# Kernel tuning notes

Measured on AMD Instinct MI355X. Metric: run time of the kernel, lower is better.

The kernel has to match this reference:

```python
import jax, jax.numpy as jnp
import numpy as np

NW, NT, F, H = 8192, 4096, 128, 128


def setup_inputs() -> dict:
    key = jax.random.key(0)
    ks = jax.random.split(key, 16)
    s = 1.0 / np.sqrt(F)
    sh = 1.0 / np.sqrt(H)
    inp = {
        "raw_worker_x": jax.random.normal(ks[0], (NW, F), jnp.float32),
        "raw_task_x": jax.random.normal(ks[1], (NT, F), jnp.float32),
        # sparse binary adjacencies (p=0.01), stored dense as the module expects
        "ww_adj": (jax.random.uniform(ks[2], (NW, NW)) < 0.01).astype(jnp.float32),
        "wt_adj": (jax.random.uniform(ks[3], (NW, NT)) < 0.01).astype(jnp.float32),
        # projections (Linear with bias), stored [in, out]
        "Wp_w": jax.random.uniform(ks[4], (F, H), jnp.float32, -s, s),
        "bp_w": jax.random.uniform(ks[5], (H,), jnp.float32, -s, s),
        "Wp_t": jax.random.uniform(ks[6], (F, H), jnp.float32, -s, s),
        "bp_t": jax.random.uniform(ks[7], (H,), jnp.float32, -s, s),
        # RGCN layer
        "W_worker": jax.random.uniform(ks[8], (H, H), jnp.float32, -sh, sh),
        "b_worker": jax.random.uniform(ks[9], (H,), jnp.float32, -sh, sh),
        "W_task": jax.random.uniform(ks[10], (H, H), jnp.float32, -sh, sh),
        "b_task": jax.random.uniform(ks[11], (H,), jnp.float32, -sh, sh),
        "W_ww": jax.random.uniform(ks[12], (H, H), jnp.float32, -sh, sh),
        "W_wt": jax.random.uniform(ks[13], (H, H), jnp.float32, -sh, sh),
        "W_tw": jax.random.uniform(ks[14], (H, H), jnp.float32, -sh, sh),
        # IGAT layer
        "W_igat": jax.random.uniform(ks[15], (H, H), jnp.float32, -sh, sh),
        "a_src": jax.random.normal(jax.random.fold_in(key, 100), (H, 1), jnp.float32) * 0.1,
        "a_dst": jax.random.normal(jax.random.fold_in(key, 101), (H, 1), jnp.float32) * 0.1,
    }
    return inp


def reference(raw_worker_x, raw_task_x, ww_adj, wt_adj,
              Wp_w, bp_w, Wp_t, bp_t,
              W_worker, b_worker, W_task, b_task,
              W_ww, W_wt, W_tw, W_igat, a_src, a_dst):
    # input projections
    h_w = jax.nn.relu(raw_worker_x @ Wp_w + bp_w)   # [NW, H]
    h_t = jax.nn.relu(raw_task_x @ Wp_t + bp_t)     # [NT, H]

    # HeteroRGCN layer
    ww_msg = ww_adj @ (h_w @ W_ww)                  # [NW, H]
    tw_msg = wt_adj @ (h_t @ W_tw)                  # [NW, H]
    wt_msg = wt_adj.T @ (h_w @ W_wt)                # [NT, H]
    h_w_rgcn = jax.nn.relu(h_w @ W_worker + b_worker + ww_msg + tw_msg)
    h_t_rgcn = jax.nn.relu(h_t @ W_task + b_task + wt_msg)

    # IGAT layer: dense masked attention over worker-worker graph
    Wh = h_w_rgcn @ W_igat                          # [NW, H]
    f_src = Wh @ a_src                              # [NW, 1]
    f_dst = Wh @ a_dst                              # [NW, 1]
    e = jax.nn.leaky_relu(f_src + f_dst.T, 0.2)     # [NW, NW]
    NEG = jnp.float32(-9e15)
    attn_logits = jnp.where(ww_adj > 0, e, NEG)
    attention = jax.nn.softmax(attn_logits, axis=-1)
    h_prime = jax.nn.elu(attention @ Wh)            # [NW, H]

    final_worker = h_prime + h_w
    final_task = h_t_rgcn + h_t
    return (final_worker, final_task)
```

## Files before the change

### kernel.cpp

```cpp
#include <hip/hip_runtime.h>

static constexpr int NWK  = 8192;
static constexpr int NTK  = 4096;
static constexpr int HD   = 128;
static constexpr int CWW  = 256;
static constexpr int CWTR = 128;
static constexpr int CWTC = 256;

typedef float  f32x4  __attribute__((ext_vector_type(4)));
typedef __bf16 bf16x8 __attribute__((ext_vector_type(8)));

__device__ __forceinline__ float b2f(unsigned short u){
  unsigned int x = ((unsigned int)u) << 16;
  return __builtin_bit_cast(float, x);
}
__device__ __forceinline__ unsigned short f2b(float x){
  return __builtin_bit_cast(unsigned short, (__bf16)x);
}
__device__ __forceinline__ float wredmax(float v){
#pragma unroll
  for(int o=32;o;o>>=1) v = fmaxf(v, __shfl_xor(v,o,64));
  return v;
}
__device__ __forceinline__ float wredsum(float v){
#pragma unroll
  for(int o=32;o;o>>=1) v += __shfl_xor(v,o,64);
  return v;
}

__global__ __launch_bounds__(256) void prepw(
    const float* s0,const float* s1,const float* s2,const float* s3,
    const float* s4,const float* s5,const float* s6,const float* s7,
    unsigned short* dst, int* fill, float* whsum){
  if(blockIdx.x < 16) fill[blockIdx.x*256 + threadIdx.x] = 0;
  if(blockIdx.x == 16 && threadIdx.x < 128) whsum[threadIdx.x] = 0.f;
  const float* srcs[8] = {s0,s1,s2,s3,s4,s5,s6,s7};
  int mat = blockIdx.x>>2, sl = blockIdx.x&3;
  const float* s = srcs[mat];
  unsigned short* d = dst + (size_t)mat*HD*HD;
  for(int idx=threadIdx.x + sl*4096; idx<(sl+1)*4096; idx+=256){
    int k = idx>>7, n = idx&127;
    d[n*HD+k] = f2b(s[idx]);
  }
}

template<int CAP>
__device__ __forceinline__ void scan_chunk(
    float4 x, int c0base, int& base, int* __restrict__ sbuf, int lane){
  bool p0=x.x>0.f, p1=x.y>0.f, p2=x.z>0.f, p3=x.w>0.f;
  unsigned long long b0=__ballot(p0),b1=__ballot(p1),b2=__ballot(p2),b3=__ballot(p3);
  unsigned long long below = (1ull<<lane)-1ull;
  int pos = base + __popcll(b0&below)+__popcll(b1&below)+__popcll(b2&below)+__popcll(b3&below);
  int c0 = c0base + lane*4;
  if(p0){ if(pos<CAP) sbuf[pos]=c0;   pos++; }
  if(p1){ if(pos<CAP) sbuf[pos]=c0+1; pos++; }
  if(p2){ if(pos<CAP) sbuf[pos]=c0+2; pos++; }
  if(p3){ if(pos<CAP) sbuf[pos]=c0+3; pos++; }
  base += __popcll(b0)+__popcll(b1)+__popcll(b2)+__popcll(b3);
}

template<bool SCATTER, int CAP>
__device__ __forceinline__ void scan_row(
    const float* __restrict__ adj, long row, int ncols,
    int* __restrict__ orow, int* __restrict__ deg,
    int* __restrict__ cidx, int* __restrict__ fill, int ccap,
    int lane, int* __restrict__ sbuf){
  const float4* arow = (const float4*)(adj + row*(long)ncols);
  int base = 0;
  const int nit = ncols>>10;
  float4 v[4], nv[4];
#pragma unroll
  for(int c=0;c<4;c++) v[c] = arow[c*64 + lane];
  for(int it=0; it<nit-1; it++){
#pragma unroll
    for(int c=0;c<4;c++) nv[c] = arow[(it+1)*256 + c*64 + lane];
#pragma unroll
    for(int c=0;c<4;c++)
      scan_chunk<CAP>(v[c], it*1024 + c*256, base, sbuf, lane);
#pragma unroll
    for(int c=0;c<4;c++) v[c] = nv[c];
  }
#pragma unroll
  for(int c=0;c<4;c++)
    scan_chunk<CAP>(v[c], (nit-1)*1024 + c*256, base, sbuf, lane);

  int d = base<CAP ? base : CAP;
  if(lane==0) deg[row] = d;
  if(CAP == 256){
    int4 q = ((const int4*)sbuf)[lane];
    ((int4*)orow)[lane] = q;
  } else {
    int2 q = ((const int2*)sbuf)[lane];
    ((int2*)orow)[lane] = q;
  }
  if(SCATTER){
    for(int k=lane; k<d; k+=64){
      int task = sbuf[k];
      int pp = atomicAdd(&fill[task], 1);
      if(pp < ccap) cidx[(long)task*ccap + pp] = (int)row;
    }
  }
}

__global__ __launch_bounds__(256) void build_all(
    const float* __restrict__ WW, const float* __restrict__ WT,
    int* __restrict__ ww_idx, int* __restrict__ ww_deg,
    int* __restrict__ wt_idx, int* __restrict__ wt_deg,
    int* __restrict__ cidx, int* __restrict__ fill){
  __shared__ int sbuf[4][CWW];
  int lane = threadIdx.x&63, w = threadIdx.x>>6;
  int b = blockIdx.x;
  if(b < NWK/4){
    long row = (long)b*4 + w;
    scan_row<false,CWW>(WW, row, NWK, ww_idx + row*CWW, ww_deg,
                        nullptr, nullptr, 0, lane, sbuf[w]);
  } else {
    long row = (long)(b - NWK/4)*4 + w;
    scan_row<true,CWTR>(WT, row, NTK, wt_idx + row*CWTR, wt_deg,
                        cidx, fill, CWTC, lane, sbuf[w]);
  }
}

__global__ __launch_bounds__(256) void kproj(
    const float* __restrict__ Xw, const float* __restrict__ Xt,
    const unsigned short* __restrict__ Wtb,
    const float* __restrict__ bp_w, const float* __restrict__ bp_t,
    unsigned short* __restrict__ h_w, unsigned short* __restrict__ h_t){
  bool task = blockIdx.x >= (NWK/32);
  const float* X = task ? Xt : Xw;
  const __bf16* Wt = (const __bf16*)(Wtb + (size_t)(task?1:0)*HD*HD);
  const float* bias = task ? bp_t : bp_w;
  unsigned short* H = task ? h_t : h_w;
  long r0 = (long)(task ? blockIdx.x-(NWK/32) : blockIdx.x)*32;

  __shared__ __bf16 As[32*HD];
  char* Ab = (char*)As;
  int t = threadIdx.x, lane = t&63, w = t>>6;
  const float4* A4 = (const float4*)(X + r0*HD);
#pragma unroll
  for(int i=0;i<4;i++){
    int id = t + i*256;
    float4 v = A4[id];
    int row = id>>5, c4 = id&31;
    int byte = row*256 + c4*8;
    ushort4 b; b.x=f2b(v.x); b.y=f2b(v.y); b.z=f2b(v.z); b.w=f2b(v.w);
    *(ushort4*)(Ab + (byte ^ ((row&7)<<4))) = b;
  }
  __syncthreads();
  f32x4 acc[2][2] = {};
  int n0 = w*32;
#pragma unroll
  for(int kk=0;kk<4;kk++){
    int kb = kk*32 + (lane>>4)*8;
    bf16x8 bf0 = *(const bf16x8*)(Wt + (n0 +      (lane&15))*HD + kb);
    bf16x8 bf1 = *(const bf16x8*)(Wt + (n0 + 16 + (lane&15))*HD + kb);
#pragma unroll
    for(int m=0;m<2;m++){
      int row = m*16 + (lane&15);
      bf16x8 af = *(const bf16x8*)(Ab + ((row*256 + kb*2) ^ ((row&7)<<4)));
      acc[m][0] = __builtin_amdgcn_mfma_f32_16x16x32_bf16(af, bf0, acc[m][0], 0,0,0);
      acc[m][1] = __builtin_amdgcn_mfma_f32_16x16x32_bf16(af, bf1, acc[m][1], 0,0,0);
    }
  }
#pragma unroll
  for(int m=0;m<2;m++)
#pragma unroll
  for(int n=0;n<2;n++){
    int col = n0 + n*16 + (lane&15);
    float bc = bias[col];
#pragma unroll
    for(int i=0;i<4;i++){
      long row = r0 + m*16 + (lane>>4)*4 + i;
      float vv = acc[m][n][i] + bc;
      vv = vv>0.f ? vv : 0.f;
      H[row*HD+col] = f2b(vv);
    }
  }
}

__device__ __forceinline__ void gather_sum(
    const unsigned short* __restrict__ tab, const int* __restrict__ ji, int d,
    int lane, float& ax, float& ay){
  int k=0;
  for(; k+3<d; k+=4){
    long j0=ji[k], j1=ji[k+1], j2=ji[k+2], j3=ji[k+3];
    ushort2 u0 = *(const ushort2*)(tab + j0*HD + lane*2);
    ushort2 u1 = *(const ushort2*)(tab + j1*HD + lane*2);
    ushort2 u2 = *(const ushort2*)(tab + j2*HD + lane*2);
    ushort2 u3 = *(const ushort2*)(tab + j3*HD + lane*2);
    ax += (b2f(u0.x)+b2f(u1.x)) + (b2f(u2.x)+b2f(u3.x));
    ay += (b2f(u0.y)+b2f(u1.y)) + (b2f(u2.y)+b2f(u3.y));
  }
  for(; k<d; ++k){
    long j0=ji[k];
    ushort2 u0 = *(const ushort2*)(tab + j0*HD + lane*2);
    ax += b2f(u0.x); ay += b2f(u0.y);
  }
}

__global__ __launch_bounds__(256) void agg(
    const unsigned short* __restrict__ h_w, const unsigned short* __restrict__ h_t,
    const int* __restrict__ wwidx, const int* __restrict__ wwdeg,
    const int* __restrict__ wtidx, const int* __restrict__ wtdeg,
    const int* __restrict__ cidx,  const int* __restrict__ fill,
    unsigned short* __restrict__ g_ww, unsigned short* __restrict__ g_tw,
    unsigned short* __restrict__ g_wt){
  int w = threadIdx.x>>6, lane = threadIdx.x&63;
  long i = (long)blockIdx.x*4 + w;
  if(i < NWK){
    float ax=0.f, ay=0.f;
    gather_sum(h_w, wwidx + i*CWW, wwdeg[i], lane, ax, ay);
    ushort2 o; o.x=f2b(ax); o.y=f2b(ay);
    *(ushort2*)(g_ww + i*HD + lane*2) = o;
    ax=0.f; ay=0.f;
    gather_sum(h_t, wtidx + i*CWTR, wtdeg[i], lane, ax, ay);
    o.x=f2b(ax); o.y=f2b(ay);
    *(ushort2*)(g_tw + i*HD + lane*2) = o;
  } else {
    long tt = i - NWK;
    float ax=0.f, ay=0.f;
    int d = fill[tt]; if(d>CWTC) d=CWTC;
    gather_sum(h_w, cidx + tt*CWTC, d, lane, ax, ay);
    ushort2 o; o.x=f2b(ax); o.y=f2b(ay);
    *(ushort2*)(g_wt + tt*HD + lane*2) = o;
  }
}

__device__ __forceinline__ void stage_bf16(char* Ab, const unsigned short* src, int t){
#pragma unroll
  for(int i=0;i<2;i++){
    int id = t + i*256;
    int row = id>>4, c8 = id&15;
    bf16x8 v = *(const bf16x8*)(src + row*HD + c8*8);
    int byte = row*256 + c8*16;
    *(bf16x8*)(Ab + (byte ^ ((row&7)<<4))) = v;
  }
}

__global__ __launch_bounds__(256) void krgcn(
    const unsigned short* __restrict__ h_w, const unsigned short* __restrict__ h_t,
    const unsigned short* __restrict__ g_ww, const unsigned short* __restrict__ g_tw,
    const unsigned short* __restrict__ g_wt,
    const unsigned short* __restrict__ Wtb,
    const float* __restrict__ b_worker, const float* __restrict__ b_task,
    const float* __restrict__ a_src, const float* __restrict__ a_dst,
    unsigned short* __restrict__ Wh, float* __restrict__ fs, float* __restrict__ fd,
    float* __restrict__ whsum, float* __restrict__ out_task){
  __shared__ __bf16 As[3][32*HD];
  __shared__ __bf16 Hs[32*HD];
  __shared__ float fsp[32][4], fdp[32][4];
  int t = threadIdx.x, lane = t&63, w = t>>6, n0 = w*32;
  bool task = blockIdx.x >= (NWK/32);

  if(!task){
    long r0 = (long)blockIdx.x*32;
    stage_bf16((char*)As[0], h_w  + r0*HD, t);
    stage_bf16((char*)As[1], g_ww + r0*HD, t);
    stage_bf16((char*)As[2], g_tw + r0*HD, t);
    __syncthreads();
    f32x4 acc[2][2] = {};
    const int slot[3] = {2,4,6};
#pragma unroll
    for(int s=0;s<3;s++){
      const __bf16* Wt = (const __bf16*)(Wtb + (size_t)slot[s]*HD*HD);
      char* Ab = (char*)As[s];
#pragma unroll
      for(int kk=0;kk<4;kk++){
        int kb = kk*32 + (lane>>4)*8;
        bf16x8 bf0 = *(const bf16x8*)(Wt + (n0 +      (lane&15))*HD + kb);
        bf16x8 bf1 = *(const bf16x8*)(Wt + (n0 + 16 + (lane&15))*HD + kb);
#pragma unroll
        for(int m=0;m<2;m++){
          int row = m*16 + (lane&15);
          bf16x8 af = *(const bf16x8*)(Ab + ((row*256 + kb*2) ^ ((row&7)<<4)));
          acc[m][0] = __builtin_amdgcn_mfma_f32_16x16x32_bf16(af, bf0, acc[m][0], 0,0,0);
          acc[m][1] = __builtin_amdgcn_mfma_f32_16x16x32_bf16(af, bf1, acc[m][1], 0,0,0);
        }
      }
    }
    char* HsB = (char*)Hs;
#pragma unroll
    for(int m=0;m<2;m++)
#pragma unroll
    for(int n=0;n<2;n++){
      int col = n0 + n*16 + (lane&15);
      float bc = b_worker[col];
#pragma unroll
      for(int i=0;i<4;i++){
        int row = m*16 + (lane>>4)*4 + i;
        float vv = acc[m][n][i] + bc;
        vv = vv>0.f ? vv : 0.f;
        int byte = row*256 + col*2;
        *(__bf16*)(HsB + (byte ^ ((row&7)<<4))) = (__bf16)vv;
      }
    }
    __syncthreads();
    f32x4 acc2[2][2] = {};
    const __bf16* Wt7 = (const __bf16*)(Wtb + (size_t)7*HD*HD);
#pragma unroll
    for(int kk=0;kk<4;kk++){
      int kb = kk*32 + (lane>>4)*8;
      bf16x8 bf0 = *(const bf16x8*)(Wt7 + (n0 +      (lane&15))*HD + kb);
      bf16x8 bf1 = *(const bf16x8*)(Wt7 + (n0 + 16 + (lane&15))*HD + kb);
#pragma unroll
      for(int m=0;m<2;m++){
        int row = m*16 + (lane&15);
        bf16x8 af = *(const bf16x8*)(HsB + ((row*256 + kb*2) ^ ((row&7)<<4)));
        acc2[m][0] = __builtin_amdgcn_mfma_f32_16x16x32_bf16(af, bf0, acc2[m][0], 0,0,0);
        acc2[m][1] = __builtin_amdgcn_mfma_f32_16x16x32_bf16(af, bf1, acc2[m][1], 0,0,0);
      }
    }
#pragma unroll
    for(int m=0;m<2;m++)
#pragma unroll
    for(int n=0;n<2;n++){
      int col = n0 + n*16 + (lane&15);
#pragma unroll
      for(int i=0;i<4;i++){
        long row = r0 + m*16 + (lane>>4)*4 + i;
        Wh[row*HD+col] = f2b(acc2[m][n][i]);
      }
    }
    float as0 = a_src[n0 + (lane&15)], as1 = a_src[n0 + 16 + (lane&15)];
    float ad0 = a_dst[n0 + (lane&15)], ad1 = a_dst[n0 + 16 + (lane&15)];
#pragma unroll
    for(int m=0;m<2;m++)
#pragma unroll
    for(int i=0;i<4;i++){
      float ps = acc2[m][0][i]*as0 + acc2[m][1][i]*as1;
      float pd = acc2[m][0][i]*ad0 + acc2[m][1][i]*ad1;
#pragma unroll
      for(int o=1;o<16;o<<=1){ ps += __shfl_xor(ps,o,64); pd += __shfl_xor(pd,o,64); }
      if((lane&15)==0){
        int row = m*16 + (lane>>4)*4 + i;
        fsp[row][w] = ps; fdp[row][w] = pd;
      }
    }
    float c0=0.f, c1=0.f;
#pragma unroll
    for(int m=0;m<2;m++)
#pragma unroll
    for(int i=0;i<4;i++){ c0 += acc2[m][0][i]; c1 += acc2[m][1][i]; }
    c0 += __shfl_xor(c0,16,64); c0 += __shfl_xor(c0,32,64);
    c1 += __shfl_xor(c1,16,64); c1 += __shfl_xor(c1,32,64);
    if(lane<16){
      atomicAdd(&whsum[n0+lane],    c0);
      atomicAdd(&whsum[n0+16+lane], c1);
    }
    __syncthreads();
    if(t < 32){
      fs[r0+t] = fsp[t][0]+fsp[t][1]+fsp[t][2]+fsp[t][3];
      fd[r0+t] = fdp[t][0]+fdp[t][1]+fdp[t][2]+fdp[t][3];
    }
  } else {
    long r0 = (long)(blockIdx.x - (NWK/32))*32;
    stage_bf16((char*)As[0], h_t  + r0*HD, t);
    stage_bf16((char*)As[1], g_wt + r0*HD, t);
    __syncthreads();
    f32x4 acc[2][2] = {};
    const int slot[2] = {3,5};
#pragma unroll
    for(int s=0;s<2;s++){
      const __bf16* Wt = (const __bf16*)(Wtb + (size_t)slot[s]*HD*HD);
      char* Ab = (char*)As[s];
#pragma unroll
      for(int kk=0;kk<4;kk++){
        int kb = kk*32 + (lane>>4)*8;
        bf16x8 bf0 = *(const bf16x8*)(Wt + (n0 +      (lane&15))*HD + kb);
        bf16x8 bf1 = *(const bf16x8*)(Wt + (n0 + 16 + (lane&15))*HD + kb);
#pragma unroll
        for(int m=0;m<2;m++){
          int row = m*16 + (lane&15);
          bf16x8 af = *(const bf16x8*)(Ab + ((row*256 + kb*2) ^ ((row&7)<<4)));
          acc[m][0] = __builtin_amdgcn_mfma_f32_16x16x32_bf16(af, bf0, acc[m][0], 0,0,0);
          acc[m][1] = __builtin_amdgcn_mfma_f32_16x16x32_bf16(af, bf1, acc[m][1], 0,0,0);
        }
      }
    }
#pragma unroll
    for(int m=0;m<2;m++)
#pragma unroll
    for(int n=0;n<2;n++){
      int col = n0 + n*16 + (lane&15);
      float bc = b_task[col];
#pragma unroll
      for(int i=0;i<4;i++){
        long row = r0 + m*16 + (lane>>4)*4 + i;
        float vv = acc[m][n][i] + bc;
        vv = vv>0.f ? vv : 0.f;
        vv += b2f(h_t[row*HD+col]);
        out_task[row*HD+col] = vv;
      }
    }
  }
}

__global__ __launch_bounds__(256) void attn(
    const unsigned short* __restrict__ Wh, const float* __restrict__ fs,
    const float* __restrict__ fd, const int* __restrict__ idx,
    const int* __restrict__ deg, const unsigned short* __restrict__ h_w,
    const float* __restrict__ whsum, float* __restrict__ out){
  __shared__ float pa[4][CWW];
  __shared__ int   pj[4][CWW];
  int w = threadIdx.x>>6, lane = threadIdx.x&63;
  long i = (long)blockIdx.x*4 + w;
  int d = deg[i];
  const int* ji = idx + i*CWW;
  float ax=0.f, ay=0.f;
  if(d > 0){
    float fsi = fs[i];
    float m = -1e30f;
    for(int k=lane;k<d;k+=64){
      int j = ji[k]; pj[w][k] = j;
      float e = fsi + fd[j];
      e = e>0.f ? e : 0.2f*e;
      pa[w][k] = e;
      m = fmaxf(m, e);
    }
    m = wredmax(m);
    float ssum = 0.f;
    for(int k=lane;k<d;k+=64){
      float e = __expf(pa[w][k]-m);
      pa[w][k] = e;
      ssum += e;
    }
    ssum = wredsum(ssum);
    float inv = 1.f/ssum;
    int k=0;
    for(; k+3<d; k+=4){
      float a0=pa[w][k], a1=pa[w][k+1], a2=pa[w][k+2], a3=pa[w][k+3];
      long j0=pj[w][k], j1=pj[w][k+1], j2=pj[w][k+2], j3=pj[w][k+3];
      ushort2 u0 = *(const ushort2*)(Wh + j0*HD + lane*2);
      ushort2 u1 = *(const ushort2*)(Wh + j1*HD + lane*2);
      ushort2 u2 = *(const ushort2*)(Wh + j2*HD + lane*2);
      ushort2 u3 = *(const ushort2*)(Wh + j3*HD + lane*2);
      ax += (a0*b2f(u0.x) + a1*b2f(u1.x)) + (a2*b2f(u2.x) + a3*b2f(u3.x));
      ay += (a0*b2f(u0.y) + a1*b2f(u1.y)) + (a2*b2f(u2.y) + a3*b2f(u3.y));
    }
    for(; k<d; ++k){
      float a0 = pa[w][k];
      long j0 = pj[w][k];
      ushort2 u0 = *(const ushort2*)(Wh + j0*HD + lane*2);
      ax += a0*b2f(u0.x);
      ay += a0*b2f(u0.y);
    }
    ax *= inv; ay *= inv;
  } else {
    ax = whsum[lane*2]   * (1.f/8192.f);
    ay = whsum[lane*2+1] * (1.f/8192.f);
  }
  ushort2 r = *(const ushort2*)(h_w + i*HD + lane*2);
  float2 o;
  o.x = (ax>0.f ? ax : __expf(ax)-1.f) + b2f(r.x);
  o.y = (ay>0.f ? ay : __expf(ay)-1.f) + b2f(r.y);
  *(float2*)(out + i*HD + lane*2) = o;
}

extern "C" void kernel_launch(void* const* d_in, const int* in_sizes, int n_in,
                              void* d_out, int out_size, void* d_ws, size_t ws_size,
                              hipStream_t stream){
  const float* Xw       = (const float*)d_in[0];
  const float* Xt       = (const float*)d_in[1];
  const float* WW       = (const float*)d_in[2];
  const float* WT       = (const float*)d_in[3];
  const float* Wp_w     = (const float*)d_in[4];
  const float* bp_w     = (const float*)d_in[5];
  const float* Wp_t     = (const float*)d_in[6];
  const float* bp_t     = (const float*)d_in[7];
  const float* W_worker = (const float*)d_in[8];
  const float* b_worker = (const float*)d_in[9];
  const float* W_task   = (const float*)d_in[10];
  const float* b_task   = (const float*)d_in[11];
  const float* W_ww     = (const float*)d_in[12];
  const float* W_wt     = (const float*)d_in[13];
  const float* W_tw     = (const float*)d_in[14];
  const float* W_igat   = (const float*)d_in[15];
  const float* a_src    = (const float*)d_in[16];
  const float* a_dst    = (const float*)d_in[17];
  float* out = (float*)d_out;

  char* p = (char*)d_ws;
  auto alloc = [&](size_t bytes)->char*{
    char* r = p; p += (bytes + 255) & ~(size_t)255; return r;
  };
  int* ww_idx  = (int*)alloc((size_t)NWK*CWW*4);
  int* wt_idx  = (int*)alloc((size_t)NWK*CWTR*4);
  int* wt_cidx = (int*)alloc((size_t)NTK*CWTC*4);
  int* ww_deg  = (int*)alloc(NWK*4);
  int* wt_deg  = (int*)alloc(NWK*4);
  int*   fill  = (int*)alloc(NTK*4);
  float* whsum = (float*)alloc(512);
  float* fs    = (float*)alloc(NWK*4);
  float* fd    = (float*)alloc(NWK*4);
  unsigned short* h_w  = (unsigned short*)alloc((size_t)NWK*HD*2);
  unsigned short* h_t  = (unsigned short*)alloc((size_t)NTK*HD*2);
  unsigned short* g_ww = (unsigned short*)alloc((size_t)NWK*HD*2);
  unsigned short* g_tw = (unsigned short*)alloc((size_t)NWK*HD*2);
  unsigned short* g_wt = (unsigned short*)alloc((size_t)NTK*HD*2);
  unsigned short* Wh   = (unsigned short*)alloc((size_t)NWK*HD*2);
  unsigned short* Wtb  = (unsigned short*)alloc((size_t)8*HD*HD*2);

  prepw<<<32,256,0,stream>>>(Wp_w, Wp_t, W_worker, W_task, W_ww, W_wt, W_tw, W_igat,
                             Wtb, fill, whsum);
  build_all<<<NWK/2,256,0,stream>>>(WW, WT, ww_idx, ww_deg, wt_idx, wt_deg, wt_cidx, fill);
  kproj<<<NWK/32 + NTK/32,256,0,stream>>>(Xw, Xt, Wtb, bp_w, bp_t, h_w, h_t);
  agg<<<(NWK+NTK)/4,256,0,stream>>>(h_w, h_t, ww_idx, ww_deg, wt_idx, wt_deg,
                                    wt_cidx, fill, g_ww, g_tw, g_wt);
  krgcn<<<NWK/32 + NTK/32,256,0,stream>>>(h_w, h_t, g_ww, g_tw, g_wt, Wtb,
                                          b_worker, b_task, a_src, a_dst,
                                          Wh, fs, fd, whsum, out + (size_t)NWK*HD);
  attn<<<NWK/4,256,0,stream>>>(Wh, fs, fd, ww_idx, ww_deg, h_w, whsum, out);
}
```

Measured before the change: 172.5 us.

## Split adjacency row scan across four waves per block

```diff
diff --git a/kernel.cpp b/kernel.cpp
--- a/kernel.cpp
+++ b/kernel.cpp
@@ -6,6 +6,8 @@
 static constexpr int CWW  = 256;
 static constexpr int CWTR = 128;
 static constexpr int CWTC = 256;
+static constexpr int QCW  = 128;
+static constexpr int QCT  = 64;
 
 typedef float  f32x4  __attribute__((ext_vector_type(4)));
 typedef __bf16 bf16x8 __attribute__((ext_vector_type(8)));
@@ -59,43 +61,35 @@
   base += __popcll(b0)+__popcll(b1)+__popcll(b2)+__popcll(b3);
 }
 
-template<bool SCATTER, int CAP>
-__device__ __forceinline__ void scan_row(
-    const float* __restrict__ adj, long row, int ncols,
+template<int NCH, int QCAP, bool SCATTER>
+__device__ __forceinline__ void scan_row_block(
+    const float* __restrict__ adj, long row, int ncols, int cap,
     int* __restrict__ orow, int* __restrict__ deg,
     int* __restrict__ cidx, int* __restrict__ fill, int ccap,
-    int lane, int* __restrict__ sbuf){
-  const float4* arow = (const float4*)(adj + row*(long)ncols);
+    int lane, int w, int (* __restrict__ sbuf)[QCW], int* __restrict__ cnts){
+  const int Q = NCH*256;
+  const float4* src = (const float4*)(adj + row*(long)ncols) + ((w*Q)>>2);
+  float4 v[NCH];
+#pragma unroll
+  for(int c=0;c<NCH;c++) v[c] = src[c*64 + lane];
   int base = 0;
-  const int nit = ncols>>10;
-  float4 v[4], nv[4];
-#pragma unroll
-  for(int c=0;c<4;c++) v[c] = arow[c*64 + lane];
-  for(int it=0; it<nit-1; it++){
-#pragma unroll
-    for(int c=0;c<4;c++) nv[c] = arow[(it+1)*256 + c*64 + lane];
-#pragma unroll
-    for(int c=0;c<4;c++)
-      scan_chunk<CAP>(v[c], it*1024 + c*256, base, sbuf, lane);
-#pragma unroll
-    for(int c=0;c<4;c++) v[c] = nv[c];
-  }
-#pragma unroll
-  for(int c=0;c<4;c++)
-    scan_chunk<CAP>(v[c], (nit-1)*1024 + c*256, base, sbuf, lane);
-
-  int d = base<CAP ? base : CAP;
-  if(lane==0) deg[row] = d;
-  if(CAP == 256){
-    int4 q = ((const int4*)sbuf)[lane];
-    ((int4*)orow)[lane] = q;
-  } else {
-    int2 q = ((const int2*)sbuf)[lane];
-    ((int2*)orow)[lane] = q;
+#pragma unroll
+  for(int c=0;c<NCH;c++)
+    scan_chunk<QCAP>(v[c], w*Q + c*256, base, sbuf[w], lane);
+  int cnt = base<QCAP ? base : QCAP;
+  if(lane==0) cnts[w] = cnt;
+  __syncthreads();
+  int c0=cnts[0], c1=cnts[1], c2=cnts[2], c3=cnts[3];
+  int off = (w>0?c0:0) + (w>1?c1:0) + (w>2?c2:0);
+  int tot = c0+c1+c2+c3;
+  if(w==0 && lane==0) deg[row] = tot<cap ? tot : cap;
+  for(int k=lane; k<cnt; k+=64){
+    int p = off+k;
+    if(p<cap) orow[p] = sbuf[w][k];
   }
   if(SCATTER){
-    for(int k=lane; k<d; k+=64){
-      int task = sbuf[k];
+    for(int k=lane; k<cnt; k+=64){
+      int task = sbuf[w][k];
       int pp = atomicAdd(&fill[task], 1);
       if(pp < ccap) cidx[(long)task*ccap + pp] = (int)row;
     }
@@ -107,17 +101,18 @@
     int* __restrict__ ww_idx, int* __restrict__ ww_deg,
     int* __restrict__ wt_idx, int* __restrict__ wt_deg,
     int* __restrict__ cidx, int* __restrict__ fill){
-  __shared__ int sbuf[4][CWW];
+  __shared__ int sbuf[4][QCW];
+  __shared__ int cnts[4];
   int lane = threadIdx.x&63, w = threadIdx.x>>6;
   int b = blockIdx.x;
-  if(b < NWK/4){
-    long row = (long)b*4 + w;
-    scan_row<false,CWW>(WW, row, NWK, ww_idx + row*CWW, ww_deg,
-                        nullptr, nullptr, 0, lane, sbuf[w]);
+  if(b < NWK){
+    long row = b;
+    scan_row_block<8,QCW,false>(WW, row, NWK, CWW, ww_idx + row*CWW, ww_deg,
+                                nullptr, nullptr, 0, lane, w, sbuf, cnts);
   } else {
-    long row = (long)(b - NWK/4)*4 + w;
-    scan_row<true,CWTR>(WT, row, NTK, wt_idx + row*CWTR, wt_deg,
-                        cidx, fill, CWTC, lane, sbuf[w]);
+    long row = b - NWK;
+    scan_row_block<4,QCT,true>(WT, row, NTK, CWTR, wt_idx + row*CWTR, wt_deg,
+                               cidx, fill, CWTC, lane, w, sbuf, cnts);
   }
 }
 
@@ -502,7 +497,8 @@
 
   prepw<<<32,256,0,stream>>>(Wp_w, Wp_t, W_worker, W_task, W_ww, W_wt, W_tw, W_igat,
                              Wtb, fill, whsum);
-  build_all<<<NWK/2,256,0,stream>>>(WW, WT, ww_idx, ww_deg, wt_idx, wt_deg, wt_cidx, fill);
+  build_all<<<NWK*2,256,0,stream>>>(WW, WT, ww_idx, ww_deg, wt_idx, wt_deg,
+                                    wt_cidx, fill);
   kproj<<<NWK/32 + NTK/32,256,0,stream>>>(Xw, Xt, Wtb, bp_w, bp_t, h_w, h_t);
   agg<<<(NWK+NTK)/4,256,0,stream>>>(h_w, h_t, ww_idx, ww_deg, wt_idx, wt_deg,
                                     wt_cidx, fill, g_ww, g_tw, g_wt);
```

After: 166.5 us. 3.5% less time.

## Split adjacency scan into bitmask compression pass and ELL build from bitmasks

Applied to the files above, without the earlier changes.

```diff
diff --git a/kernel.cpp b/kernel.cpp
--- a/kernel.cpp
+++ b/kernel.cpp
@@ -44,66 +44,84 @@
   }
 }
 
-template<int CAP>
-__device__ __forceinline__ void scan_chunk(
-    float4 x, int c0base, int& base, int* __restrict__ sbuf, int lane){
-  bool p0=x.x>0.f, p1=x.y>0.f, p2=x.z>0.f, p3=x.w>0.f;
-  unsigned long long b0=__ballot(p0),b1=__ballot(p1),b2=__ballot(p2),b3=__ballot(p3);
-  unsigned long long below = (1ull<<lane)-1ull;
-  int pos = base + __popcll(b0&below)+__popcll(b1&below)+__popcll(b2&below)+__popcll(b3&below);
-  int c0 = c0base + lane*4;
-  if(p0){ if(pos<CAP) sbuf[pos]=c0;   pos++; }
-  if(p1){ if(pos<CAP) sbuf[pos]=c0+1; pos++; }
-  if(p2){ if(pos<CAP) sbuf[pos]=c0+2; pos++; }
-  if(p3){ if(pos<CAP) sbuf[pos]=c0+3; pos++; }
-  base += __popcll(b0)+__popcll(b1)+__popcll(b2)+__popcll(b3);
-}
-
-template<bool SCATTER, int CAP>
-__device__ __forceinline__ void scan_row(
-    const float* __restrict__ adj, long row, int ncols,
-    int* __restrict__ orow, int* __restrict__ deg,
-    int* __restrict__ cidx, int* __restrict__ fill, int ccap,
-    int lane, int* __restrict__ sbuf){
-  const float4* arow = (const float4*)(adj + row*(long)ncols);
-  int base = 0;
-  const int nit = ncols>>10;
-  float4 v[4], nv[4];
-#pragma unroll
-  for(int c=0;c<4;c++) v[c] = arow[c*64 + lane];
-  for(int it=0; it<nit-1; it++){
-#pragma unroll
-    for(int c=0;c<4;c++) nv[c] = arow[(it+1)*256 + c*64 + lane];
-#pragma unroll
-    for(int c=0;c<4;c++)
-      scan_chunk<CAP>(v[c], it*1024 + c*256, base, sbuf, lane);
-#pragma unroll
-    for(int c=0;c<4;c++) v[c] = nv[c];
-  }
-#pragma unroll
-  for(int c=0;c<4;c++)
-    scan_chunk<CAP>(v[c], (nit-1)*1024 + c*256, base, sbuf, lane);
-
-  int d = base<CAP ? base : CAP;
-  if(lane==0) deg[row] = d;
-  if(CAP == 256){
-    int4 q = ((const int4*)sbuf)[lane];
-    ((int4*)orow)[lane] = q;
-  } else {
-    int2 q = ((const int2*)sbuf)[lane];
-    ((int2*)orow)[lane] = q;
-  }
-  if(SCATTER){
-    for(int k=lane; k<d; k+=64){
-      int task = sbuf[k];
-      int pp = atomicAdd(&fill[task], 1);
-      if(pp < ccap) cidx[(long)task*ccap + pp] = (int)row;
-    }
-  }
-}
-
-__global__ __launch_bounds__(256) void build_all(
+__device__ __forceinline__ void mask_chunk(
+    const float4* __restrict__ src4, size_t c,
+    unsigned long long* __restrict__ mask, int lane){
+  float4 v = src4[c*64 + lane];
+  unsigned int nib = (v.x>0.f?1u:0u)|(v.y>0.f?2u:0u)|(v.z>0.f?4u:0u)|(v.w>0.f?8u:0u);
+  unsigned int t;
+  t = __shfl_xor(nib,1,64);  nib = (lane&1) ? (t|(nib<<4))  : (nib|(t<<4));
+  t = __shfl_xor(nib,2,64);  nib = (lane&2) ? (t|(nib<<8))  : (nib|(t<<8));
+  t = __shfl_xor(nib,4,64);  nib = (lane&4) ? (t|(nib<<16)) : (nib|(t<<16));
+  t = __shfl_xor(nib,8,64);
+  unsigned int lo = (lane&8)? t : nib;
+  unsigned int hi = (lane&8)? nib : t;
+  if((lane&15)==0){
+    unsigned long long wv = (unsigned long long)lo | ((unsigned long long)hi<<32);
+    mask[c*4 + (lane>>4)] = wv;
+  }
+}
+
+__global__ __launch_bounds__(256) void maskify(
     const float* __restrict__ WW, const float* __restrict__ WT,
+    unsigned long long* __restrict__ mask_ww,
+    unsigned long long* __restrict__ mask_wt){
+  const int NW = 8192;
+  int wid = (blockIdx.x*256 + threadIdx.x)>>6;
+  int lane = threadIdx.x&63;
+  const float4* ww4 = (const float4*)WW;
+  const float4* wt4 = (const float4*)WT;
+  for(int i=0;i<32;i+=4){
+    size_t c[4];
+    float4 v[4];
+#pragma unroll
+    for(int u=0;u<4;u++){ c[u] = (size_t)wid + (size_t)(i+u)*NW; }
+#pragma unroll
+    for(int u=0;u<4;u++){ v[u] = ww4[c[u]*64 + lane]; }
+#pragma unroll
+    for(int u=0;u<4;u++){
+      unsigned int nib = (v[u].x>0.f?1u:0u)|(v[u].y>0.f?2u:0u)|(v[u].z>0.f?4u:0u)|(v[u].w>0.f?8u:0u);
+      unsigned int t;
+      t = __shfl_xor(nib,1,64);  nib = (lane&1) ? (t|(nib<<4))  : (nib|(t<<4));
+      t = __shfl_xor(nib,2,64);  nib = (lane&2) ? (t|(nib<<8))  : (nib|(t<<8));
+      t = __shfl_xor(nib,4,64);  nib = (lane&4) ? (t|(nib<<16)) : (nib|(t<<16));
+      t = __shfl_xor(nib,8,64);
+      unsigned int lo = (lane&8)? t : nib;
+      unsigned int hi = (lane&8)? nib : t;
+      if((lane&15)==0){
+        mask_ww[c[u]*4 + (lane>>4)] =
+          (unsigned long long)lo | ((unsigned long long)hi<<32);
+      }
+    }
+  }
+  for(int i=0;i<16;i+=4){
+    size_t c[4];
+    float4 v[4];
+#pragma unroll
+    for(int u=0;u<4;u++){ c[u] = (size_t)wid + (size_t)(i+u)*NW; }
+#pragma unroll
+    for(int u=0;u<4;u++){ v[u] = wt4[c[u]*64 + lane]; }
+#pragma unroll
+    for(int u=0;u<4;u++){
+      unsigned int nib = (v[u].x>0.f?1u:0u)|(v[u].y>0.f?2u:0u)|(v[u].z>0.f?4u:0u)|(v[u].w>0.f?8u:0u);
+      unsigned int t;
+      t = __shfl_xor(nib,1,64);  nib = (lane&1) ? (t|(nib<<4))  : (nib|(t<<4));
+      t = __shfl_xor(nib,2,64);  nib = (lane&2) ? (t|(nib<<8))  : (nib|(t<<8));
+      t = __shfl_xor(nib,4,64);  nib = (lane&4) ? (t|(nib<<16)) : (nib|(t<<16));
+      t = __shfl_xor(nib,8,64);
+      unsigned int lo = (lane&8)? t : nib;
+      unsigned int hi = (lane&8)? nib : t;
+      if((lane&15)==0){
+        mask_wt[c[u]*4 + (lane>>4)] =
+          (unsigned long long)lo | ((unsigned long long)hi<<32);
+      }
+    }
+  }
+}
+
+__global__ __launch_bounds__(256) void build_ell(
+    const unsigned long long* __restrict__ mask_ww,
+    const unsigned long long* __restrict__ mask_wt,
     int* __restrict__ ww_idx, int* __restrict__ ww_deg,
     int* __restrict__ wt_idx, int* __restrict__ wt_deg,
     int* __restrict__ cidx, int* __restrict__ fill){
@@ -111,13 +129,43 @@
   int lane = threadIdx.x&63, w = threadIdx.x>>6;
   int b = blockIdx.x;
   if(b < NWK/4){
-    long row = (long)b*4 + w;
-    scan_row<false,CWW>(WW, row, NWK, ww_idx + row*CWW, ww_deg,
-                        nullptr, nullptr, 0, lane, sbuf[w]);
+    int row = b*4 + w;
+    const unsigned long long* mrow = mask_ww + (size_t)row*128;
+    unsigned long long w0 = mrow[lane*2], w1 = mrow[lane*2+1];
+    int cnt = __popcll(w0) + __popcll(w1);
+    int run = cnt;
+#pragma unroll
+    for(int o=1;o<64;o<<=1){ int tt=__shfl_up(run,o,64); if(lane>=o) run+=tt; }
+    int ex = run - cnt;
+    int tot = __shfl(run, 63, 64);
+    if(lane==0) ww_deg[row] = tot<CWW ? tot : CWW;
+    int pos = ex, base = lane*128;
+    while(w0){ int bit=__builtin_ctzll(w0); w0 &= w0-1; if(pos<CWW) sbuf[w][pos]=base+bit; pos++; }
+    base += 64;
+    while(w1){ int bit=__builtin_ctzll(w1); w1 &= w1-1; if(pos<CWW) sbuf[w][pos]=base+bit; pos++; }
+    int4 q = ((const int4*)sbuf[w])[lane];
+    ((int4*)(ww_idx + (size_t)row*CWW))[lane] = q;
   } else {
-    long row = (long)(b - NWK/4)*4 + w;
-    scan_row<true,CWTR>(WT, row, NTK, wt_idx + row*CWTR, wt_deg,
-                        cidx, fill, CWTC, lane, sbuf[w]);
+    int row = (b - NWK/4)*4 + w;
+    const unsigned long long* mrow = mask_wt + (size_t)row*64;
+    unsigned long long w0 = mrow[lane];
+    int cnt = __popcll(w0);
+    int run = cnt;
+#pragma unroll
+    for(int o=1;o<64;o<<=1){ int tt=__shfl_up(run,o,64); if(lane>=o) run+=tt; }
+    int ex = run - cnt;
+    int tot = __shfl(run, 63, 64);
+    int d = tot<CWTR ? tot : CWTR;
+    if(lane==0) wt_deg[row] = d;
+    int pos = ex, base = lane*64;
+    while(w0){ int bit=__builtin_ctzll(w0); w0 &= w0-1; if(pos<CWTR) sbuf[w][pos]=base+bit; pos++; }
+    int2 q = ((const int2*)sbuf[w])[lane];
+    ((int2*)(wt_idx + (size_t)row*CWTR))[lane] = q;
+    for(int k=lane; k<d; k+=64){
+      int task = sbuf[w][k];
+      int pp = atomicAdd(&fill[task], 1);
+      if(pp < CWTC) cidx[(size_t)task*CWTC + pp] = row;
+    }
   }
 }
 
@@ -483,6 +531,8 @@
   auto alloc = [&](size_t bytes)->char*{
     char* r = p; p += (bytes + 255) & ~(size_t)255; return r;
   };
+  unsigned long long* mask_ww = (unsigned long long*)alloc((size_t)NWK*NWK/8);
+  unsigned long long* mask_wt = (unsigned long long*)alloc((size_t)NWK*NTK/8);
   int* ww_idx  = (int*)alloc((size_t)NWK*CWW*4);
   int* wt_idx  = (int*)alloc((size_t)NWK*CWTR*4);
   int* wt_cidx = (int*)alloc((size_t)NTK*CWTC*4);
@@ -502,7 +552,9 @@
 
   prepw<<<32,256,0,stream>>>(Wp_w, Wp_t, W_worker, W_task, W_ww, W_wt, W_tw, W_igat,
                              Wtb, fill, whsum);
-  build_all<<<NWK/2,256,0,stream>>>(WW, WT, ww_idx, ww_deg, wt_idx, wt_deg, wt_cidx, fill);
+  maskify<<<2048,256,0,stream>>>(WW, WT, mask_ww, mask_wt);
+  build_ell<<<NWK/2,256,0,stream>>>(mask_ww, mask_wt, ww_idx, ww_deg,
+                                    wt_idx, wt_deg, wt_cidx, fill);
   kproj<<<NWK/32 + NTK/32,256,0,stream>>>(Xw, Xt, Wtb, bp_w, bp_t, h_w, h_t);
   agg<<<(NWK+NTK)/4,256,0,stream>>>(h_w, h_t, ww_idx, ww_deg, wt_idx, wt_deg,
                                     wt_cidx, fill, g_ww, g_tw, g_wt);
```

Result: slower. 205.3 us (+19.0%).
